# Optimization experiments

Hardware: AMD Instinct MI355X
Metric: run time of the kernel (lower is better)

Reference implementation:

```python
import jax, jax.numpy as jnp
import numpy as np

ALPHA = 0.2  # LeakyReLU negative slope
NEG_INF = -9e15


def setup_inputs() -> dict:
    key = jax.random.key(0)
    k1, k2, k3, k4 = jax.random.split(key, 4)
    B, N, F_in, F_out = 8, 2048, 256, 128
    h = jax.random.normal(k1, (B, N, F_in), dtype=jnp.float32)
    adj = jax.random.randint(k2, (B, N, N), 0, 2, dtype=jnp.int32)
    # xavier_uniform with gain=1.414
    def xavier(k, shape, gain=1.414):
        fan_in, fan_out = shape[0], shape[1]
        limit = gain * np.sqrt(6.0 / (fan_in + fan_out))
        return jax.random.uniform(k, shape, jnp.float32, -limit, limit)
    W = xavier(k3, (F_in, F_out))
    a = xavier(k4, (2 * F_out, 1))
    return {"h": h, "adj": adj, "W": W, "a": a}


def reference(h, adj, W, a):
    # h: [B,N,F_in], adj: [B,N,N], W: [F_in,F_out], a: [2*F_out,1]
    Wh = jnp.einsum('bnf,fe->bne', h, W)  # [B,N,E]
    E = Wh.shape[-1]
    a_src, a_dst = a[:E, 0], a[E:, 0]
    # e[b,i,j] = leakyrelu(Wh[b,i].a_src + Wh[b,j].a_dst)  (additive decomposition
    # of a @ concat(Wh_i, Wh_j) -- same math, no [B,N,N,2E] intermediate)
    s_src = Wh @ a_src  # [B,N]
    s_dst = Wh @ a_dst  # [B,N]
    e = jax.nn.leaky_relu(s_src[:, :, None] + s_dst[:, None, :], negative_slope=ALPHA)
    e = jnp.where(adj > 0, e, NEG_INF)
    attention = jax.nn.softmax(e, axis=2)  # [B,N,N]
    # dropout p=0.0 / eval mode -> identity
    h_prime = jnp.einsum('bij,bje->bie', attention, Wh)
    return jax.nn.elu(h_prime)  # concat=True
```

## Files before the change

kernel.cpp:

```cpp
#include <hip/hip_runtime.h>
#include <hip/hip_bf16.h>

#define GAT_ALPHA 0.2f
#define LOG2E 1.4426950408889634f

typedef float f32x4 __attribute__((ext_vector_type(4)));
typedef int   i32x4 __attribute__((ext_vector_type(4)));
typedef short bf16x8 __attribute__((ext_vector_type(8)));

static constexpr int Nn  = 2048;
static constexpr int FIN = 256;
static constexpr int FO  = 128;

static __device__ __forceinline__ unsigned short f2bf(float x) {
    __hip_bfloat16 h = __float2bfloat16(x);
    return __builtin_bit_cast(unsigned short, h);
}
static __device__ __forceinline__ float bf2f(unsigned short u) {
    unsigned int v = ((unsigned int)u) << 16;
    return __builtin_bit_cast(float, v);
}

__global__ __launch_bounds__(256) void gat_prep(
        const float* __restrict__ W, const float* __restrict__ a,
        float* __restrict__ wa, unsigned int* __restrict__ md_key)
{
    __shared__ float pr[32][8];
    __shared__ float pd[32][8];
    const int t = threadIdx.x;
    const int kl = t >> 3, seg = t & 7;
    const int k = blockIdx.x * 32 + kl;
    float ps = 0.f, pv = 0.f;
    const float* wr = W + (size_t)k * FO + seg * 16;
    #pragma unroll
    for (int f = 0; f < 16; f += 4) {
        f32x4 wv = *(const f32x4*)(wr + f);
        f32x4 as = *(const f32x4*)(a + seg * 16 + f);
        f32x4 ad = *(const f32x4*)(a + FO + seg * 16 + f);
        ps += wv[0]*as[0] + wv[1]*as[1] + wv[2]*as[2] + wv[3]*as[3];
        pv += wv[0]*ad[0] + wv[1]*ad[1] + wv[2]*ad[2] + wv[3]*ad[3];
    }
    pr[kl][seg] = ps; pd[kl][seg] = pv;
    __syncthreads();
    if (t < 32) {
        float s = 0.f, d = 0.f;
        #pragma unroll
        for (int j = 0; j < 8; ++j) { s += pr[t][j]; d += pd[t][j]; }
        wa[blockIdx.x * 32 + t]       = s;
        wa[256 + blockIdx.x * 32 + t] = d;
    }
    if (blockIdx.x == 0 && t < 8) md_key[t] = 0u;
}

__global__ __launch_bounds__(256) void gat_wh(
        const float* __restrict__ h, const float* __restrict__ W,
        const float* __restrict__ wa, unsigned short* __restrict__ Wp,
        float* __restrict__ s_src, float* __restrict__ s_dst,
        unsigned int* __restrict__ md_key)
{
    __shared__ unsigned short WT[FO][264];
    __shared__ float wal[512];
    __shared__ float sred[64][4][2];
    __shared__ float red64[64];
    const int t  = threadIdx.x;
    const int b  = blockIdx.x & 7;
    const int n0 = (blockIdx.x >> 3) << 6;

    if (t < 128) *(f32x4*)&wal[t * 4] = *(const f32x4*)&wa[t * 4];
    #pragma unroll
    for (int c = 0; c < 32; ++c) {
        int flat = c * 1024 + t * 4;
        int k = flat >> 7, f = flat & 127;
        f32x4 wv = *(const f32x4*)&W[flat];
        WT[f + 0][k] = f2bf(wv[0]);
        WT[f + 1][k] = f2bf(wv[1]);
        WT[f + 2][k] = f2bf(wv[2]);
        WT[f + 3][k] = f2bf(wv[3]);
    }
    __syncthreads();

    {
        const int row = t >> 2, seg = t & 3;
        const float* hp  = h + ((size_t)(b * Nn + n0 + row)) * FIN + seg * 64;
        const float* was = &wal[seg * 64];
        const float* wad = &wal[256 + seg * 64];
        float ps = 0.f, pv = 0.f;
        #pragma unroll
        for (int j = 0; j < 64; j += 4) {
            f32x4 hv = *(const f32x4*)(hp + j);
            f32x4 sv = *(const f32x4*)(was + j);
            f32x4 dv = *(const f32x4*)(wad + j);
            ps += hv[0]*sv[0] + hv[1]*sv[1] + hv[2]*sv[2] + hv[3]*sv[3];
            pv += hv[0]*dv[0] + hv[1]*dv[1] + hv[2]*dv[2] + hv[3]*dv[3];
        }
        sred[row][seg][0] = ps;
        sred[row][seg][1] = pv;
    }
    __syncthreads();
    if (t < 64) {
        float s = sred[t][0][0] + sred[t][1][0] + sred[t][2][0] + sred[t][3][0];
        float d = sred[t][0][1] + sred[t][1][1] + sred[t][2][1] + sred[t][3][1];
        s_src[b * Nn + n0 + t] = s;
        s_dst[b * Nn + n0 + t] = d;
        red64[t] = d;
    }
    __syncthreads();
    if (t < 16) red64[t] = fmaxf(fmaxf(red64[t], red64[t + 16]),
                                 fmaxf(red64[t + 32], red64[t + 48]));
    __syncthreads();
    if (t == 0) {
        float m = red64[0];
        #pragma unroll
        for (int j = 1; j < 16; ++j) m = fmaxf(m, red64[j]);
        unsigned int bits = __builtin_bit_cast(unsigned int, m);
        unsigned int key  = (bits & 0x80000000u) ? ~bits : (bits | 0x80000000u);
        atomicMax(md_key + b, key);
    }

    const int w = t >> 6, lane = t & 63, n16 = lane & 15, quad = lane >> 4;
    const float* ha = h + ((size_t)(b * Nn + n0 + w * 16 + n16)) * FIN + quad * 8;
    f32x4 acc[8] = {};
    #pragma unroll
    for (int ks = 0; ks < 8; ++ks) {
        f32x4 h0 = *(const f32x4*)(ha + ks * 32);
        f32x4 h1 = *(const f32x4*)(ha + ks * 32 + 4);
        bf16x8 af;
        af[0] = (short)f2bf(h0[0]); af[1] = (short)f2bf(h0[1]);
        af[2] = (short)f2bf(h0[2]); af[3] = (short)f2bf(h0[3]);
        af[4] = (short)f2bf(h1[0]); af[5] = (short)f2bf(h1[1]);
        af[6] = (short)f2bf(h1[2]); af[7] = (short)f2bf(h1[3]);
        #pragma unroll
        for (int nt = 0; nt < 8; ++nt) {
            bf16x8 bfr = *(const bf16x8*)&WT[nt * 16 + n16][ks * 32 + quad * 8];
            acc[nt] = __builtin_amdgcn_mfma_f32_16x16x32_bf16(af, bfr, acc[nt], 0, 0, 0);
        }
    }
    {
        const int v      = (n0 >> 5) + (w >> 1);
        const int quad_p = ((w & 1) << 1) + (quad >> 1);
        const int eoff   = (quad & 1) << 2;
        #pragma unroll
        for (int nt = 0; nt < 8; ++nt) {
            ushort4 pk;
            pk.x = f2bf(acc[nt][0]); pk.y = f2bf(acc[nt][1]);
            pk.z = f2bf(acc[nt][2]); pk.w = f2bf(acc[nt][3]);
            size_t idx = ((((size_t)(b << 6) + v) * 8 + nt) * 64 + quad_p * 16 + n16) * 8 + eoff;
            *(ushort4*)&Wp[idx] = pk;
        }
    }
}

__global__ __launch_bounds__(256, 4) void gat_attn(
        const int* __restrict__ adj, const unsigned short* __restrict__ Wp,
        const float* __restrict__ s_src, const float* __restrict__ s_dst,
        const unsigned int* __restrict__ md_key, float* __restrict__ out)
{
    constexpr int AS = 132;
    __shared__ __align__(16) float accbuf[2 * 16 * AS];
    __shared__ float l_red[16];

    const int t = threadIdx.x, w = t >> 6, lane = t & 63;
    const int n16 = lane & 15, quad = lane >> 4;
    const int b  = blockIdx.x & 7;
    const int i0 = (blockIdx.x >> 3) << 4;

    if (t < 16) l_red[t] = 0.f;
    __syncthreads();

    const unsigned int key = md_key[b];
    const unsigned int mb  = (key & 0x80000000u) ? (key ^ 0x80000000u) : ~key;
    const float mdb = __builtin_bit_cast(float, mb);

    const float ssr = s_src[b * Nn + i0 + n16];
    const float tm  = ssr + mdb;
    const float mi  = fmaxf(tm, GAT_ALPHA * tm) * LOG2E;
    const float sL  = ssr * LOG2E;

    const int jw = (w << 5) + (quad << 3);
    const int* ap    = adj + ((size_t)(b * Nn + i0 + n16)) * Nn + jw;
    const float* dptr = s_dst + b * Nn + jw;
    const unsigned short* wp = Wp + ((size_t)b << 18) + ((size_t)w << 12) + (lane << 3);

    f32x4 acc[8] = {};
    float ls = 0.f;

    i32x4 pa0 = *(const i32x4*)(ap);
    i32x4 pa1 = *(const i32x4*)(ap + 4);

    for (int s = 0; s < 16; ++s) {
        const int j0 = s << 7;
        const unsigned short* wts = wp + (s << 14);
        bf16x8 bfr[8];
        #pragma unroll
        for (int nt = 0; nt < 8; ++nt)
            bfr[nt] = *(const bf16x8*)(wts + (nt << 9));
        f32x4 d0 = *(const f32x4*)(dptr + j0);
        f32x4 d1 = *(const f32x4*)(dptr + j0 + 4);
        const int jn = (s < 15) ? (j0 + 128) : 0;
        i32x4 na0 = *(const i32x4*)(ap + jn);
        i32x4 na1 = *(const i32x4*)(ap + jn + 4);

        bf16x8 af;
        #pragma unroll
        for (int j = 0; j < 4; ++j) {
            float u  = __builtin_fmaf(d0[j], LOG2E, sL);
            float lr = fmaxf(u, GAT_ALPHA * u);
            float e  = __builtin_amdgcn_exp2f(lr - mi);
            e = (pa0[j] > 0) ? e : 0.f;
            unsigned short us = f2bf(e);
            ls += bf2f(us); af[j] = (short)us;
        }
        #pragma unroll
        for (int j = 0; j < 4; ++j) {
            float u  = __builtin_fmaf(d1[j], LOG2E, sL);
            float lr = fmaxf(u, GAT_ALPHA * u);
            float e  = __builtin_amdgcn_exp2f(lr - mi);
            e = (pa1[j] > 0) ? e : 0.f;
            unsigned short us = f2bf(e);
            ls += bf2f(us); af[4 + j] = (short)us;
        }
        #pragma unroll
        for (int nt = 0; nt < 8; ++nt)
            acc[nt] = __builtin_amdgcn_mfma_f32_16x16x32_bf16(af, bfr[nt], acc[nt], 0, 0, 0);
        pa0 = na0; pa1 = na1;
    }

    ls += __shfl_xor(ls, 16); ls += __shfl_xor(ls, 32);
    if (quad == 0) atomicAdd(&l_red[n16], ls);

    float* slot = accbuf + (size_t)(w & 1) * 16 * AS;
    if (w < 2) {
        #pragma unroll
        for (int nt = 0; nt < 8; ++nt)
            #pragma unroll
            for (int rr = 0; rr < 4; ++rr)
                slot[(quad * 4 + rr) * AS + nt * 16 + n16] = acc[nt][rr];
    }
    __syncthreads();
    if (w >= 2) {
        #pragma unroll
        for (int nt = 0; nt < 8; ++nt)
            #pragma unroll
            for (int rr = 0; rr < 4; ++rr)
                slot[(quad * 4 + rr) * AS + nt * 16 + n16] += acc[nt][rr];
    }
    __syncthreads();
    float* ob = out + ((size_t)(b * Nn + i0)) * FO;
    #pragma unroll
    for (int c = 0; c < 2; ++c) {
        int flat = c * 1024 + t * 4;
        int m = flat >> 7, f = flat & 127;
        f32x4 v0 = *(const f32x4*)&accbuf[(size_t)m * AS + f];
        f32x4 v1 = *(const f32x4*)&accbuf[(size_t)16 * AS + m * AS + f];
        float l = l_red[m];
        f32x4 o;
        #pragma unroll
        for (int j = 0; j < 4; ++j) {
            float x = (v0[j] + v1[j]) / l;
            o[j] = x > 0.f ? x : expm1f(x);
        }
        *(f32x4*)&ob[(size_t)m * FO + f] = o;
    }
}

extern "C" void kernel_launch(void* const* d_in, const int* in_sizes, int n_in,
                              void* d_out, int out_size, void* d_ws, size_t ws_size,
                              hipStream_t stream)
{
    const float* h   = (const float*)d_in[0];
    const int*   adj = (const int*)d_in[1];
    const float* W   = (const float*)d_in[2];
    const float* a   = (const float*)d_in[3];
    float* out = (float*)d_out;

    char* ws = (char*)d_ws;
    unsigned short* Wp  = (unsigned short*)ws;
    float* s_src        = (float*)(ws + 4194304);
    float* s_dst        = (float*)(ws + 4259840);
    float* wa           = (float*)(ws + 4325376);
    unsigned int* md_key= (unsigned int*)(ws + 4327424);

    hipLaunchKernelGGL(gat_prep, dim3(8),    dim3(256), 0, stream, W, a, wa, md_key);
    hipLaunchKernelGGL(gat_wh,   dim3(256),  dim3(256), 0, stream, h, W, wa, Wp, s_src, s_dst, md_key);
    hipLaunchKernelGGL(gat_attn, dim3(1024), dim3(256), 0, stream, adj, Wp, s_src, s_dst, md_key, out);
}
```

Before: 257.5 us.

## Stage Wh tiles in double-buffered LDS shared across 64-row attention blocks

The attention kernel now processes 64 query rows per block with 512 threads (8 waves: 4 row groups × 2 j-windows) instead of 16 rows with 256 threads. Each 64-column slice of the packed bf16 Wh is loaded cooperatively into a double-buffered LDS tile and reused by all four row groups. Previously every wave streamed its Wh fragments straight from global memory. This cuts global/L2 traffic for Wh by about 4x, at the cost of a __syncthreads per step, more LDS use and a grid of only 256 blocks.

```diff
diff --git a/kernel.cpp b/kernel.cpp
--- a/kernel.cpp
+++ b/kernel.cpp
@@ -150,53 +150,64 @@
     }
 }
 
-__global__ __launch_bounds__(256, 4) void gat_attn(
+__global__ __launch_bounds__(512, 2) void gat_attn(
         const int* __restrict__ adj, const unsigned short* __restrict__ Wp,
         const float* __restrict__ s_src, const float* __restrict__ s_dst,
         const unsigned int* __restrict__ md_key, float* __restrict__ out)
 {
     constexpr int AS = 132;
-    __shared__ __align__(16) float accbuf[2 * 16 * AS];
-    __shared__ float l_red[16];
+    __shared__ __align__(16) float smem_f[64 * AS];
+    __shared__ float l_red[64];
+    unsigned short* ldsw = (unsigned short*)smem_f;
 
     const int t = threadIdx.x, w = t >> 6, lane = t & 63;
     const int n16 = lane & 15, quad = lane >> 4;
+    const int rg = w & 3, jwin = w >> 2;
     const int b  = blockIdx.x & 7;
-    const int i0 = (blockIdx.x >> 3) << 4;
-
-    if (t < 16) l_red[t] = 0.f;
-    __syncthreads();
+    const int i0 = (blockIdx.x >> 3) << 6;
+
+    if (t < 64) l_red[t] = 0.f;
 
     const unsigned int key = md_key[b];
     const unsigned int mb  = (key & 0x80000000u) ? (key ^ 0x80000000u) : ~key;
     const float mdb = __builtin_bit_cast(float, mb);
 
-    const float ssr = s_src[b * Nn + i0 + n16];
+    const int row = i0 + rg * 16 + n16;
+    const float ssr = s_src[b * Nn + row];
     const float tm  = ssr + mdb;
     const float mi  = fmaxf(tm, GAT_ALPHA * tm) * LOG2E;
     const float sL  = ssr * LOG2E;
 
-    const int jw = (w << 5) + (quad << 3);
-    const int* ap    = adj + ((size_t)(b * Nn + i0 + n16)) * Nn + jw;
+    const int jw = (jwin << 5) + (quad << 3);
+    const int* ap    = adj + ((size_t)(b * Nn + row)) * Nn + jw;
     const float* dptr = s_dst + b * Nn + jw;
-    const unsigned short* wp = Wp + ((size_t)b << 18) + ((size_t)w << 12) + (lane << 3);
+    const unsigned short* wsrc = Wp + ((size_t)b << 18) + (t << 4);
 
     f32x4 acc[8] = {};
     float ls = 0.f;
 
+    {
+        f32x4 g0 = *(const f32x4*)(wsrc);
+        f32x4 g1 = *(const f32x4*)(wsrc + 8);
+        *(f32x4*)&ldsw[(t << 4)]     = g0;
+        *(f32x4*)&ldsw[(t << 4) + 8] = g1;
+    }
     i32x4 pa0 = *(const i32x4*)(ap);
     i32x4 pa1 = *(const i32x4*)(ap + 4);
-
-    for (int s = 0; s < 16; ++s) {
-        const int j0 = s << 7;
-        const unsigned short* wts = wp + (s << 14);
-        bf16x8 bfr[8];
-        #pragma unroll
-        for (int nt = 0; nt < 8; ++nt)
-            bfr[nt] = *(const bf16x8*)(wts + (nt << 9));
+    __syncthreads();
+
+    for (int s = 0; s < 32; ++s) {
+        const int j0  = s << 6;
+        const int cur = s & 1, nxt = cur ^ 1;
         f32x4 d0 = *(const f32x4*)(dptr + j0);
         f32x4 d1 = *(const f32x4*)(dptr + j0 + 4);
-        const int jn = (s < 15) ? (j0 + 128) : 0;
+        f32x4 g0, g1;
+        if (s < 31) {
+            const unsigned short* src = wsrc + (s + 1) * 8192;
+            g0 = *(const f32x4*)(src);
+            g1 = *(const f32x4*)(src + 8);
+        }
+        const int jn = (s < 31) ? ((s + 1) << 6) : 0;
         i32x4 na0 = *(const i32x4*)(ap + jn);
         i32x4 na1 = *(const i32x4*)(ap + jn + 4);
 
@@ -219,44 +230,54 @@
             unsigned short us = f2bf(e);
             ls += bf2f(us); af[4 + j] = (short)us;
         }
-        #pragma unroll
-        for (int nt = 0; nt < 8; ++nt)
-            acc[nt] = __builtin_amdgcn_mfma_f32_16x16x32_bf16(af, bfr[nt], acc[nt], 0, 0, 0);
+
+        const unsigned short* bbase = &ldsw[cur * 8192 + (jwin << 12) + (lane << 3)];
+        #pragma unroll
+        for (int nt = 0; nt < 8; ++nt) {
+            bf16x8 bfr = *(const bf16x8*)(bbase + (nt << 9));
+            acc[nt] = __builtin_amdgcn_mfma_f32_16x16x32_bf16(af, bfr, acc[nt], 0, 0, 0);
+        }
+
+        if (s < 31) {
+            *(f32x4*)&ldsw[nxt * 8192 + (t << 4)]     = g0;
+            *(f32x4*)&ldsw[nxt * 8192 + (t << 4) + 8] = g1;
+        }
         pa0 = na0; pa1 = na1;
+        __syncthreads();
     }
 
     ls += __shfl_xor(ls, 16); ls += __shfl_xor(ls, 32);
-    if (quad == 0) atomicAdd(&l_red[n16], ls);
-
-    float* slot = accbuf + (size_t)(w & 1) * 16 * AS;
-    if (w < 2) {
+    if (quad == 0) atomicAdd(&l_red[rg * 16 + n16], ls);
+
+    float* slotp = smem_f + (size_t)(rg * 16) * AS;
+    if (jwin == 0) {
         #pragma unroll
         for (int nt = 0; nt < 8; ++nt)
             #pragma unroll
             for (int rr = 0; rr < 4; ++rr)
-                slot[(quad * 4 + rr) * AS + nt * 16 + n16] = acc[nt][rr];
-    }
-    __syncthreads();
-    if (w >= 2) {
+                slotp[(quad * 4 + rr) * AS + nt * 16 + n16] = acc[nt][rr];
+    }
+    __syncthreads();
+    if (jwin == 1) {
         #pragma unroll
         for (int nt = 0; nt < 8; ++nt)
             #pragma unroll
             for (int rr = 0; rr < 4; ++rr)
-                slot[(quad * 4 + rr) * AS + nt * 16 + n16] += acc[nt][rr];
-    }
-    __syncthreads();
+                slotp[(quad * 4 + rr) * AS + nt * 16 + n16] += acc[nt][rr];
+    }
+    __syncthreads();
+
     float* ob = out + ((size_t)(b * Nn + i0)) * FO;
     #pragma unroll
-    for (int c = 0; c < 2; ++c) {
-        int flat = c * 1024 + t * 4;
+    for (int c = 0; c < 4; ++c) {
+        int flat = c * 2048 + t * 4;
         int m = flat >> 7, f = flat & 127;
-        f32x4 v0 = *(const f32x4*)&accbuf[(size_t)m * AS + f];
-        f32x4 v1 = *(const f32x4*)&accbuf[(size_t)16 * AS + m * AS + f];
+        f32x4 v = *(const f32x4*)&smem_f[(size_t)m * AS + f];
         float l = l_red[m];
         f32x4 o;
         #pragma unroll
         for (int j = 0; j < 4; ++j) {
-            float x = (v0[j] + v1[j]) / l;
+            float x = v[j] / l;
             o[j] = x > 0.f ? x : expm1f(x);
         }
         *(f32x4*)&ob[(size_t)m * FO + f] = o;
@@ -280,7 +301,7 @@
     float* wa           = (float*)(ws + 4325376);
     unsigned int* md_key= (unsigned int*)(ws + 4327424);
 
-    hipLaunchKernelGGL(gat_prep, dim3(8),    dim3(256), 0, stream, W, a, wa, md_key);
-    hipLaunchKernelGGL(gat_wh,   dim3(256),  dim3(256), 0, stream, h, W, wa, Wp, s_src, s_dst, md_key);
-    hipLaunchKernelGGL(gat_attn, dim3(1024), dim3(256), 0, stream, adj, Wp, s_src, s_dst, md_key, out);
-}
+    hipLaunchKernelGGL(gat_prep, dim3(8),   dim3(256), 0, stream, W, a, wa, md_key);
+    hipLaunchKernelGGL(gat_wh,   dim3(256), dim3(256), 0, stream, h, W, wa, Wp, s_src, s_dst, md_key);
+    hipLaunchKernelGGL(gat_attn, dim3(256), dim3(512), 0, stream, adj, Wp, s_src, s_dst, md_key, out);
+}
```

New measurement: 256.3 us. No clear change (-0.5%).

## Process 64 query rows per block to reuse Wh fragments across row groups

Applied to the files above, without the earlier changes.

Each attention block now handles 64 rows (four 16-row groups) with 8 waves splitting the key dimension, so every Wh B-fragment loaded feeds four MFMAs instead of one. The cross-wave reduction grows to four LDS partial buffers. The cost is a much larger register and LDS footprint, limiting residency to one block per CU. The software prefetch of adjacency tiles is also dropped.

```diff
diff --git a/kernel.cpp b/kernel.cpp
--- a/kernel.cpp
+++ b/kernel.cpp
@@ -150,113 +150,134 @@
     }
 }
 
-__global__ __launch_bounds__(256, 4) void gat_attn(
+__global__ __launch_bounds__(512, 1) void gat_attn(
         const int* __restrict__ adj, const unsigned short* __restrict__ Wp,
         const float* __restrict__ s_src, const float* __restrict__ s_dst,
         const unsigned int* __restrict__ md_key, float* __restrict__ out)
 {
     constexpr int AS = 132;
-    __shared__ __align__(16) float accbuf[2 * 16 * AS];
-    __shared__ float l_red[16];
+    __shared__ __align__(16) float red4[4][64 * AS];
+    __shared__ float l_red[64];
 
     const int t = threadIdx.x, w = t >> 6, lane = t & 63;
     const int n16 = lane & 15, quad = lane >> 4;
     const int b  = blockIdx.x & 7;
-    const int i0 = (blockIdx.x >> 3) << 4;
-
-    if (t < 16) l_red[t] = 0.f;
+    const int i0 = (blockIdx.x >> 3) << 6;
+
+    if (t < 64) l_red[t] = 0.f;
     __syncthreads();
 
     const unsigned int key = md_key[b];
-    const unsigned int mb  = (key & 0x80000000u) ? (key ^ 0x80000000u) : ~key;
-    const float mdb = __builtin_bit_cast(float, mb);
-
-    const float ssr = s_src[b * Nn + i0 + n16];
-    const float tm  = ssr + mdb;
-    const float mi  = fmaxf(tm, GAT_ALPHA * tm) * LOG2E;
-    const float sL  = ssr * LOG2E;
-
-    const int jw = (w << 5) + (quad << 3);
-    const int* ap    = adj + ((size_t)(b * Nn + i0 + n16)) * Nn + jw;
-    const float* dptr = s_dst + b * Nn + jw;
-    const unsigned short* wp = Wp + ((size_t)b << 18) + ((size_t)w << 12) + (lane << 3);
-
-    f32x4 acc[8] = {};
-    float ls = 0.f;
-
-    i32x4 pa0 = *(const i32x4*)(ap);
-    i32x4 pa1 = *(const i32x4*)(ap + 4);
-
-    for (int s = 0; s < 16; ++s) {
-        const int j0 = s << 7;
-        const unsigned short* wts = wp + (s << 14);
+    const unsigned int mb_ = (key & 0x80000000u) ? (key ^ 0x80000000u) : ~key;
+    const float mdb = __builtin_bit_cast(float, mb_);
+
+    float mi[4], sL[4];
+    #pragma unroll
+    for (int ig = 0; ig < 4; ++ig) {
+        float ssr = s_src[b * Nn + i0 + ig * 16 + n16];
+        float tm  = ssr + mdb;
+        mi[ig] = fmaxf(tm, GAT_ALPHA * tm) * LOG2E;
+        sL[ig] = ssr * LOG2E;
+    }
+
+    const int jq = (w << 5) + (quad << 3);
+    const int* ab = adj + ((size_t)(b * Nn + i0 + n16)) * Nn + jq;
+    const float* dptr = s_dst + b * Nn + jq;
+    const unsigned short* wpb = Wp + ((size_t)b << 18) + (w << 12) + (lane << 3);
+
+    f32x4 acc[4][8] = {};
+    float ls[4] = {0.f, 0.f, 0.f, 0.f};
+
+    for (int s = 0; s < 8; ++s) {
+        const int j0 = s << 8;
+        i32x4 a0[4], a1[4];
+        #pragma unroll
+        for (int ig = 0; ig < 4; ++ig) {
+            const int* ar = ab + (size_t)(ig << 4) * Nn;
+            a0[ig] = *(const i32x4*)(ar + j0);
+            a1[ig] = *(const i32x4*)(ar + j0 + 4);
+        }
         bf16x8 bfr[8];
         #pragma unroll
         for (int nt = 0; nt < 8; ++nt)
-            bfr[nt] = *(const bf16x8*)(wts + (nt << 9));
+            bfr[nt] = *(const bf16x8*)(wpb + (s << 15) + (nt << 9));
         f32x4 d0 = *(const f32x4*)(dptr + j0);
         f32x4 d1 = *(const f32x4*)(dptr + j0 + 4);
-        const int jn = (s < 15) ? (j0 + 128) : 0;
-        i32x4 na0 = *(const i32x4*)(ap + jn);
-        i32x4 na1 = *(const i32x4*)(ap + jn + 4);
-
-        bf16x8 af;
-        #pragma unroll
-        for (int j = 0; j < 4; ++j) {
-            float u  = __builtin_fmaf(d0[j], LOG2E, sL);
-            float lr = fmaxf(u, GAT_ALPHA * u);
-            float e  = __builtin_amdgcn_exp2f(lr - mi);
-            e = (pa0[j] > 0) ? e : 0.f;
-            unsigned short us = f2bf(e);
-            ls += bf2f(us); af[j] = (short)us;
-        }
-        #pragma unroll
-        for (int j = 0; j < 4; ++j) {
-            float u  = __builtin_fmaf(d1[j], LOG2E, sL);
-            float lr = fmaxf(u, GAT_ALPHA * u);
-            float e  = __builtin_amdgcn_exp2f(lr - mi);
-            e = (pa1[j] > 0) ? e : 0.f;
-            unsigned short us = f2bf(e);
-            ls += bf2f(us); af[4 + j] = (short)us;
-        }
-        #pragma unroll
-        for (int nt = 0; nt < 8; ++nt)
-            acc[nt] = __builtin_amdgcn_mfma_f32_16x16x32_bf16(af, bfr[nt], acc[nt], 0, 0, 0);
-        pa0 = na0; pa1 = na1;
-    }
-
-    ls += __shfl_xor(ls, 16); ls += __shfl_xor(ls, 32);
-    if (quad == 0) atomicAdd(&l_red[n16], ls);
-
-    float* slot = accbuf + (size_t)(w & 1) * 16 * AS;
-    if (w < 2) {
+
+        bf16x8 af[4];
+        #pragma unroll
+        for (int ig = 0; ig < 4; ++ig) {
+            #pragma unroll
+            for (int j = 0; j < 4; ++j) {
+                {   float u  = __builtin_fmaf(d0[j], LOG2E, sL[ig]);
+                    float lr = fmaxf(u, GAT_ALPHA * u);
+                    float e  = __builtin_amdgcn_exp2f(lr - mi[ig]);
+                    e = (a0[ig][j] > 0) ? e : 0.f;
+                    unsigned short us = f2bf(e);
+                    ls[ig] += bf2f(us); af[ig][j] = (short)us; }
+                {   float u  = __builtin_fmaf(d1[j], LOG2E, sL[ig]);
+                    float lr = fmaxf(u, GAT_ALPHA * u);
+                    float e  = __builtin_amdgcn_exp2f(lr - mi[ig]);
+                    e = (a1[ig][j] > 0) ? e : 0.f;
+                    unsigned short us = f2bf(e);
+                    ls[ig] += bf2f(us); af[ig][4 + j] = (short)us; }
+            }
+        }
         #pragma unroll
         for (int nt = 0; nt < 8; ++nt)
             #pragma unroll
-            for (int rr = 0; rr < 4; ++rr)
-                slot[(quad * 4 + rr) * AS + nt * 16 + n16] = acc[nt][rr];
-    }
-    __syncthreads();
-    if (w >= 2) {
-        #pragma unroll
-        for (int nt = 0; nt < 8; ++nt)
+            for (int ig = 0; ig < 4; ++ig)
+                acc[ig][nt] = __builtin_amdgcn_mfma_f32_16x16x32_bf16(af[ig], bfr[nt], acc[ig][nt], 0, 0, 0);
+    }
+
+    #pragma unroll
+    for (int ig = 0; ig < 4; ++ig) {
+        ls[ig] += __shfl_xor(ls[ig], 16);
+        ls[ig] += __shfl_xor(ls[ig], 32);
+    }
+    if (quad == 0) {
+        #pragma unroll
+        for (int ig = 0; ig < 4; ++ig)
+            atomicAdd(&l_red[ig * 16 + n16], ls[ig]);
+    }
+
+    if (w < 4) {
+        float* slot = red4[w];
+        #pragma unroll
+        for (int ig = 0; ig < 4; ++ig)
             #pragma unroll
-            for (int rr = 0; rr < 4; ++rr)
-                slot[(quad * 4 + rr) * AS + nt * 16 + n16] += acc[nt][rr];
-    }
-    __syncthreads();
+            for (int nt = 0; nt < 8; ++nt)
+                #pragma unroll
+                for (int rr = 0; rr < 4; ++rr)
+                    slot[(size_t)(ig * 16 + quad * 4 + rr) * AS + nt * 16 + n16] = acc[ig][nt][rr];
+    }
+    __syncthreads();
+    if (w >= 4) {
+        float* slot = red4[w - 4];
+        #pragma unroll
+        for (int ig = 0; ig < 4; ++ig)
+            #pragma unroll
+            for (int nt = 0; nt < 8; ++nt)
+                #pragma unroll
+                for (int rr = 0; rr < 4; ++rr)
+                    slot[(size_t)(ig * 16 + quad * 4 + rr) * AS + nt * 16 + n16] += acc[ig][nt][rr];
+    }
+    __syncthreads();
+
     float* ob = out + ((size_t)(b * Nn + i0)) * FO;
     #pragma unroll
-    for (int c = 0; c < 2; ++c) {
-        int flat = c * 1024 + t * 4;
+    for (int c = 0; c < 4; ++c) {
+        int flat = c * 2048 + t * 4;
         int m = flat >> 7, f = flat & 127;
-        f32x4 v0 = *(const f32x4*)&accbuf[(size_t)m * AS + f];
-        f32x4 v1 = *(const f32x4*)&accbuf[(size_t)16 * AS + m * AS + f];
+        f32x4 v0 = *(const f32x4*)&red4[0][(size_t)m * AS + f];
+        f32x4 v1 = *(const f32x4*)&red4[1][(size_t)m * AS + f];
+        f32x4 v2 = *(const f32x4*)&red4[2][(size_t)m * AS + f];
+        f32x4 v3 = *(const f32x4*)&red4[3][(size_t)m * AS + f];
         float l = l_red[m];
         f32x4 o;
         #pragma unroll
         for (int j = 0; j < 4; ++j) {
-            float x = (v0[j] + v1[j]) / l;
+            float x = (v0[j] + v1[j] + v2[j] + v3[j]) / l;
             o[j] = x > 0.f ? x : expm1f(x);
         }
         *(f32x4*)&ob[(size_t)m * FO + f] = o;
@@ -280,7 +301,7 @@
     float* wa           = (float*)(ws + 4325376);
     unsigned int* md_key= (unsigned int*)(ws + 4327424);
 
-    hipLaunchKernelGGL(gat_prep, dim3(8),    dim3(256), 0, stream, W, a, wa, md_key);
-    hipLaunchKernelGGL(gat_wh,   dim3(256),  dim3(256), 0, stream, h, W, wa, Wp, s_src, s_dst, md_key);
-    hipLaunchKernelGGL(gat_attn, dim3(1024), dim3(256), 0, stream, adj, Wp, s_src, s_dst, md_key, out);
-}
+    hipLaunchKernelGGL(gat_prep, dim3(8),   dim3(256), 0, stream, W, a, wa, md_key);
+    hipLaunchKernelGGL(gat_wh,   dim3(256), dim3(256), 0, stream, h, W, wa, Wp, s_src, s_dst, md_key);
+    hipLaunchKernelGGL(gat_attn, dim3(256), dim3(512), 0, stream, adj, Wp, s_src, s_dst, md_key, out);
+}
```

Result: faster. 235.5 us (-8.5%).
